# Performance work log

Hardware: AMD Instinct MI355X
Metric: run time of the kernel (lower is better)

## Reference

```python
import jax, jax.numpy as jnp
import numpy as np

THR1 = 0.8     # lif1 threshold
THR2 = 1.0     # lif2 (Synaptic) default threshold
ALPHA2 = 0.9   # Synaptic alpha (not learnable, use_stdp=False)
BETA2 = 0.8    # Synaptic beta
SLOPE = 25.0   # snntorch fast_sigmoid default slope

@jax.custom_vjp
def fast_sigmoid_spike(x):
    return (x > 0).astype(x.dtype)

def _fs_fwd(x):
    return fast_sigmoid_spike(x), x

def _fs_bwd(x, g):
    return (g / (SLOPE * jnp.abs(x) + 1.0) ** 2,)

fast_sigmoid_spike.defvjp(_fs_fwd, _fs_bwd)

@jax.custom_vjp
def atan_spike(x):  # snntorch default ATan surrogate, alpha=2.0
    return (x > 0).astype(x.dtype)

def _at_fwd(x):
    return atan_spike(x), x

def _at_bwd(x, g):
    return (g / (1.0 + (jnp.pi * x) ** 2),)

atan_spike.defvjp(_at_fwd, _at_bwd)

def setup_inputs() -> dict:
    key = jax.random.key(0)
    k = jax.random.split(key, 6)
    B, S, V, H, E, T = 16, 16, 16000, 512, 256, 20
    x = jax.random.randint(k[0], (B, S), 0, V)
    embed_w = jax.random.normal(k[1], (V, E), dtype=jnp.float32)  # torch Embedding ~ N(0,1)
    fc1_w = jax.random.normal(k[2], (H, E), dtype=jnp.float32) / np.sqrt(E)
    fc1_b = jax.random.normal(k[3], (H,), dtype=jnp.float32) / np.sqrt(E)
    fc2_w = jax.random.normal(k[4], (V, H), dtype=jnp.float32) / np.sqrt(H)
    fc2_b = jax.random.normal(k[5], (V,), dtype=jnp.float32) / np.sqrt(H)
    beta1 = jnp.float32(0.85)  # learnable Leaky beta
    return {"x": x, "embed_w": embed_w, "fc1_w": fc1_w, "fc1_b": fc1_b,
            "fc2_w": fc2_w, "fc2_b": fc2_b, "beta1": beta1, "time_steps": T}

def reference(x, embed_w, fc1_w, fc1_b, fc2_w, fc2_b, beta1, time_steps):
    B, S = x.shape
    H = fc1_w.shape[0]
    V = fc2_w.shape[0]
    emb = embed_w[x]                       # [B, S, 256]
    b1 = jnp.clip(beta1, 0.0, 1.0)
    mem1 = jnp.zeros((B, H), emb.dtype)
    syn2 = jnp.zeros((B, V), emb.dtype)
    mem2 = jnp.zeros((B, V), emb.dtype)

    def token_step(carry, emb_t):          # emb_t: [B, 256]
        mem1, syn2, mem2 = carry
        cur1 = emb_t @ fc1_w.T + fc1_b     # identical every inner step (hoisted)

        def inner(c, _):
            m1, s2, m2, _ = c
            reset = fast_sigmoid_spike(m1 - THR1)          # reset from previous mem
            m1 = b1 * m1 + cur1 - reset * THR1             # Leaky, subtract reset
            spk1 = fast_sigmoid_spike(m1 - THR1)
            cur2 = spk1 @ fc2_w.T + fc2_b                  # [B, V]
            s2 = ALPHA2 * s2 + cur2                        # Synaptic, reset='none'
            m2 = BETA2 * m2 + s2
            spk2 = atan_spike(m2 - THR2)
            return (m1, s2, m2, spk2), None

        (mem1, syn2, mem2, spk2), _ = jax.lax.scan(
            inner, (mem1, syn2, mem2, jnp.zeros_like(mem2)), None, length=time_steps)
        return (mem1, syn2, mem2), spk2    # keep last spk2 of inner loop

    (mem1, syn2, mem2), outs = jax.lax.scan(
        token_step, (mem1, syn2, mem2), jnp.swapaxes(emb, 0, 1))  # scan over seq
    out = jnp.transpose(outs, (1, 0, 2))   # [B, S, V]
    return out, mem1, syn2, mem2
```

## Files before the change

kernel.cpp:

```cpp
#include <hip/hip_runtime.h>

#define Bdim 16
#define Sdim 16
#define Edim 256
#define Hdim 512
#define Vdim 16000
#define THR1f 0.8f
#define THR2f 1.0f

typedef unsigned int   u32;
typedef unsigned short u16;
typedef __attribute__((ext_vector_type(8))) short bf16x8;
typedef __attribute__((ext_vector_type(4))) float f32x4;

__device__ __forceinline__ u16 f2bf(float f) {
  u32 u = __float_as_uint(f);
  return (u16)((u + 0x7FFFu + ((u >> 16) & 1u)) >> 16);
}
__device__ __forceinline__ u32 pack2(float a, float b) {
  return (u32)f2bf(a) | ((u32)f2bf(b) << 16);
}
__device__ __forceinline__ void gload16(const void* g, const void* lds) {
  __builtin_amdgcn_global_load_lds(
      (const __attribute__((address_space(1))) u32*)g,
      (__attribute__((address_space(3))) u32*)lds, 16, 0, 0);
}

__global__ __launch_bounds__(256) void snn_cur1(
    const int* __restrict__ x, const float* __restrict__ embed_w,
    const float* __restrict__ fc1_w, const float* __restrict__ fc1_b,
    float* __restrict__ cur1)
{
  __shared__ __align__(16) float As[64][68];
  __shared__ __align__(16) float Ws[64][68];
  __shared__ int sidx[64];
  const int tid = threadIdx.x;
  const int n0 = blockIdx.x * 64, r0 = blockIdx.y * 64;
  const int tx = tid & 15, ty = tid >> 4;

  if (tid < 64) {
    const int r1 = r0 + tid;
    sidx[tid] = x[(r1 & 15) * Sdim + (r1 >> 4)];
  }

  float acc[4][4] = {{0.f}};
  for (int k0 = 0; k0 < Edim; k0 += 64) {
    __syncthreads();
#pragma unroll
    for (int i = 0; i < 16; ++i) {
      const int k = tid + i * 256;
      const int rr = k >> 6, j = k & 63;
      As[j][rr] = embed_w[(size_t)sidx[rr] * Edim + k0 + j];
      Ws[j][rr] = fc1_w[(size_t)(n0 + rr) * Edim + k0 + j];
    }
    __syncthreads();
#pragma unroll
    for (int j = 0; j < 64; ++j) {
      const float4 av = *(const float4*)&As[j][ty * 4];
      const float4 wv = *(const float4*)&Ws[j][tx * 4];
      const float a[4] = {av.x, av.y, av.z, av.w};
      const float w[4] = {wv.x, wv.y, wv.z, wv.w};
#pragma unroll
      for (int i = 0; i < 4; ++i)
#pragma unroll
        for (int jj = 0; jj < 4; ++jj)
          acc[i][jj] = fmaf(a[i], w[jj], acc[i][jj]);
    }
  }
#pragma unroll
  for (int i = 0; i < 4; ++i) {
    float4 o;
    o.x = acc[i][0] + fc1_b[n0 + tx * 4 + 0];
    o.y = acc[i][1] + fc1_b[n0 + tx * 4 + 1];
    o.z = acc[i][2] + fc1_b[n0 + tx * 4 + 2];
    o.w = acc[i][3] + fc1_b[n0 + tx * 4 + 3];
    *(float4*)&cur1[(size_t)(r0 + ty * 4 + i) * Hdim + n0 + tx * 4] = o;
  }
}

__global__ __launch_bounds__(256) void snn_rec(
    const float* __restrict__ cur1, const float* __restrict__ beta1p,
    const int* __restrict__ tsp, u16* __restrict__ Ab,
    float* __restrict__ mem1)
{
  const int id = blockIdx.x * 256 + threadIdx.x;
  const int b = id >> 9, h = id & 511;
  const float b1 = fminf(fmaxf(beta1p[0], 0.f), 1.f);
  const int T = tsp[0];

  double w9T = 1.0, w8T = 1.0;
  for (int i = 0; i < T; ++i) { w9T *= 0.9; w8T *= 0.8; }

  float m1 = 0.f;
  for (int t = 0; t < Sdim; ++t) {
    const float cur = cur1[(size_t)(t * Bdim + b) * Hdim + h];
    double p9 = w9T, p8 = w8T;
    float cs = 0.f, cm = 0.f;
    for (int u = 0; u < T; ++u) {
      const float reset = (m1 > THR1f) ? THR1f : 0.f;
      m1 = b1 * m1 + cur - reset;
      if (m1 > THR1f) {
        cs += (float)(p9 * (10.0 / 9.0));
        cm += (float)(10.0 * (p9 - p8));
      }
      p9 *= (10.0 / 9.0);
      p8 *= 1.25;
    }
    const size_t r = (size_t)(t * Bdim + b) * 2;
    Ab[r * Hdim + h]       = f2bf(cs);
    Ab[(r + 1) * Hdim + h] = f2bf(cm);
  }
  mem1[b * Hdim + h] = m1;
}

__global__ __launch_bounds__(256) void snn_fused(
    const u16* __restrict__ Ab, const float* __restrict__ W,
    const float* __restrict__ fc2_b, const int* __restrict__ tsp,
    float* __restrict__ out, float* __restrict__ syn2, float* __restrict__ mem2)
{
  __shared__ __align__(16) u16 As[512 * 64];
  __shared__ __align__(16) u16 Bs[64 * 64];
  const int tid  = threadIdx.x;
  const int lane = tid & 63;
  const int wid  = tid >> 6;
  const int v0   = blockIdx.x * 64;

  f32x4 acc[32];
#pragma unroll
  for (int i = 0; i < 32; ++i)
#pragma unroll
    for (int e = 0; e < 4; ++e) acc[i][e] = 0.f;

  char* AsB = (char*)As;
  char* BsB = (char*)Bs;

  const int brow = tid >> 2;
  const int bkc  = (tid & 3) * 16;
  const int bswz = (brow & 7) << 4;

  for (int k0 = 0; k0 < Hdim; k0 += 64) {
#pragma unroll
    for (int rnd = 0; rnd < 16; ++rnd) {
      const int base = rnd * 4096 + wid * 1024;
      const int flat = base + lane * 16;
      const int row  = flat >> 7;
      const int cl   = (flat & 127) ^ ((row & 7) << 4);
      gload16(Ab + ((size_t)row << 9) + k0 + (cl >> 1), AsB + base);
    }
    {
      const float4* wp =
          (const float4*)&W[(size_t)(v0 + brow) * Hdim + k0 + bkc];
      const float4 w0 = wp[0], w1 = wp[1], w2 = wp[2], w3 = wp[3];
      uint4 o0, o1;
      o0.x = pack2(w0.x, w0.y); o0.y = pack2(w0.z, w0.w);
      o0.z = pack2(w1.x, w1.y); o0.w = pack2(w1.z, w1.w);
      o1.x = pack2(w2.x, w2.y); o1.y = pack2(w2.z, w2.w);
      o1.z = pack2(w3.x, w3.y); o1.w = pack2(w3.z, w3.w);
      const int cb = bkc * 2;
      *(uint4*)(BsB + brow * 128 + (cb ^ bswz)) = o0;
      *(uint4*)(BsB + brow * 128 + ((cb + 16) ^ bswz)) = o1;
    }
    __syncthreads();
#pragma unroll
    for (int kk = 0; kk < 2; ++kk) {
      const int cbase = kk * 64 + ((lane >> 4) << 4);
      const int br = wid * 16 + (lane & 15);
      const bf16x8 bfr =
          *(const bf16x8*)(BsB + br * 128 + (cbase ^ ((br & 7) << 4)));
#pragma unroll
      for (int mi = 0; mi < 32; ++mi) {
        const int ar = mi * 16 + (lane & 15);
        const bf16x8 af =
            *(const bf16x8*)(AsB + ar * 128 + (cbase ^ ((ar & 7) << 4)));
        acc[mi] = __builtin_amdgcn_mfma_f32_16x16x32_bf16(af, bfr, acc[mi],
                                                          0, 0, 0);
      }
    }
    __syncthreads();
  }

  const int T = tsp[0];
  double p9 = 1.0, p8 = 1.0;
  for (int i = 0; i < T; ++i) { p9 *= 0.9; p8 *= 0.8; }
  const float Ps  = (float)p9;
  const float Pm  = (float)p8;
  const float Pms = (float)(0.9 * 10.0 * (p9 - p8));
  const float Sws = (float)(10.0 * (1.0 - p9));
  const float Swm = (float)(10.0 * (9.0 * (1.0 - p9) - 4.0 * (1.0 - p8)));

  const int g = lane >> 4;
  const int v = v0 + wid * 16 + (lane & 15);
  const float bb  = fc2_b[v];
  const float bbs = bb * Sws;
  const float bbm = bb * Swm;

#pragma unroll
  for (int hi = 0; hi < 2; ++hi) {
#pragma unroll
    for (int j = 0; j < 2; ++j) {
      const int b = hi * 8 + 2 * g + j;
      float s2 = 0.f, m2 = 0.f;
#pragma unroll
      for (int t = 0; t < Sdim; ++t) {
        const float gs = acc[2 * t + hi][2 * j];
        const float gm = acc[2 * t + hi][2 * j + 1];
        const float m2n = Pm * m2 + Pms * s2 + gm + bbm;
        s2 = Ps * s2 + gs + bbs;
        m2 = m2n;
        out[((size_t)b * Sdim + t) * Vdim + v] = (m2 > THR2f) ? 1.f : 0.f;
      }
      syn2[(size_t)b * Vdim + v] = s2;
      mem2[(size_t)b * Vdim + v] = m2;
    }
  }
}

extern "C" void kernel_launch(void* const* d_in, const int* in_sizes, int n_in,
                              void* d_out, int out_size, void* d_ws, size_t ws_size,
                              hipStream_t stream) {
  const int*   x       = (const int*)d_in[0];
  const float* embed_w = (const float*)d_in[1];
  const float* fc1_w   = (const float*)d_in[2];
  const float* fc1_b   = (const float*)d_in[3];
  const float* fc2_w   = (const float*)d_in[4];
  const float* fc2_b   = (const float*)d_in[5];
  const float* beta1   = (const float*)d_in[6];
  const int*   tsteps  = (const int*)d_in[7];

  float* out  = (float*)d_out;
  float* mem1 = out + (size_t)Bdim * Sdim * Vdim;
  float* syn2 = mem1 + (size_t)Bdim * Hdim;
  float* mem2 = syn2 + (size_t)Bdim * Vdim;

  float* cur1 = (float*)d_ws;
  u16*   Ab   = (u16*)((char*)d_ws + 524288);

  snn_cur1<<<dim3(Hdim / 64, (Sdim * Bdim) / 64), 256, 0, stream>>>(
      x, embed_w, fc1_w, fc1_b, cur1);
  snn_rec<<<(Bdim * Hdim) / 256, 256, 0, stream>>>(cur1, beta1, tsteps, Ab, mem1);
  snn_fused<<<Vdim / 64, 256, 0, stream>>>(Ab, fc2_w, fc2_b, tsteps,
                                           out, syn2, mem2);
}
```

Before: 156.3 us.

## Double-buffer fused GEMM, use 32x32 MFMA with 8 waves splitting M

Rewrites the fused fc2 GEMM kernel to use 512 threads (8 waves), each computing a 64x64 M-slice with 32x32x16 bf16 MFMAs. A and B tiles are double-buffered in LDS so the next k-chunk's global loads overlap the current MFMAs, and the per-iteration barrier count drops to one. Because time steps are now split across waves, the synaptic recurrence epilogue is serialized through LDS state handoff across 8 barrier stages. The aim is to cut register pressure from the 32 accumulators and hide load latency, but LDS use roughly doubles and the epilogue becomes sequential across waves.

Result: no change. 157.7 us (+0.9%).

```diff
diff --git a/kernel.cpp b/kernel.cpp
--- a/kernel.cpp
+++ b/kernel.cpp
@@ -10,8 +10,8 @@
 
 typedef unsigned int   u32;
 typedef unsigned short u16;
-typedef __attribute__((ext_vector_type(8))) short bf16x8;
-typedef __attribute__((ext_vector_type(4))) float f32x4;
+typedef __attribute__((ext_vector_type(8)))  short bf16x8;
+typedef __attribute__((ext_vector_type(16))) float f32x16;
 
 __device__ __forceinline__ u16 f2bf(float f) {
   u32 u = __float_as_uint(f);
@@ -113,70 +113,97 @@
   mem1[b * Hdim + h] = m1;
 }
 
-__global__ __launch_bounds__(256) void snn_fused(
+__global__ __launch_bounds__(512, 2) void snn_fused(
     const u16* __restrict__ Ab, const float* __restrict__ W,
     const float* __restrict__ fc2_b, const int* __restrict__ tsp,
     float* __restrict__ out, float* __restrict__ syn2, float* __restrict__ mem2)
 {
-  __shared__ __align__(16) u16 As[512 * 64];
-  __shared__ __align__(16) u16 Bs[64 * 64];
+  __shared__ __align__(16) u16 AsBuf[2][512 * 64];
+  __shared__ __align__(16) u16 BsBuf[2][64 * 64];
+  __shared__ float2 stbuf[16 * 64];
   const int tid  = threadIdx.x;
   const int lane = tid & 63;
-  const int wid  = tid >> 6;
+  const int wm   = tid >> 6;
   const int v0   = blockIdx.x * 64;
 
-  f32x4 acc[32];
-#pragma unroll
-  for (int i = 0; i < 32; ++i)
-#pragma unroll
-    for (int e = 0; e < 4; ++e) acc[i][e] = 0.f;
-
-  char* AsB = (char*)As;
-  char* BsB = (char*)Bs;
-
-  const int brow = tid >> 2;
-  const int bkc  = (tid & 3) * 16;
-  const int bswz = (brow & 7) << 4;
-
+  f32x16 acc[2][2];
+#pragma unroll
+  for (int mi = 0; mi < 2; ++mi)
+#pragma unroll
+    for (int nj = 0; nj < 2; ++nj)
+#pragma unroll
+      for (int e = 0; e < 16; ++e) acc[mi][nj][e] = 0.f;
+
+  const int brow = tid >> 3;
+  const int bk8  = (tid & 7) * 8;
+  const int bdst = brow * 128 + (((tid & 7) * 16) ^ ((brow & 7) << 4));
+
+#define STAGE_A(buf, k0s)                                                    \
+  {                                                                          \
+    _Pragma("unroll")                                                        \
+    for (int rnd = 0; rnd < 8; ++rnd) {                                      \
+      const int base = rnd * 8192 + (wm << 10);            \
+      const int flat = base + lane * 16;                                     \
+      const int row  = flat >> 7;                                            \
+      const int cl   = (flat & 127) ^ ((row & 7) << 4);                      \
+      gload16(Ab + ((size_t)row << 9) + (k0s) + (cl >> 1),                   \
+              (char*)AsBuf[buf] + base);                                     \
+    }                                                                        \
+  }
+
+  STAGE_A(0, 0);
+  {
+    const float4* wp = (const float4*)&W[(size_t)(v0 + brow) * Hdim + bk8];
+    const float4 wa = wp[0], wb = wp[1];
+    uint4 o;
+    o.x = pack2(wa.x, wa.y); o.y = pack2(wa.z, wa.w);
+    o.z = pack2(wb.x, wb.y); o.w = pack2(wb.z, wb.w);
+    *(uint4*)((char*)BsBuf[0] + bdst) = o;
+  }
+  __syncthreads();
+
+  int c = 0;
   for (int k0 = 0; k0 < Hdim; k0 += 64) {
-#pragma unroll
-    for (int rnd = 0; rnd < 16; ++rnd) {
-      const int base = rnd * 4096 + wid * 1024;
-      const int flat = base + lane * 16;
-      const int row  = flat >> 7;
-      const int cl   = (flat & 127) ^ ((row & 7) << 4);
-      gload16(Ab + ((size_t)row << 9) + k0 + (cl >> 1), AsB + base);
-    }
-    {
+    float4 wa, wb;
+    const bool pf = (k0 + 64 < Hdim);
+    if (pf) {
+      STAGE_A(c ^ 1, k0 + 64);
       const float4* wp =
-          (const float4*)&W[(size_t)(v0 + brow) * Hdim + k0 + bkc];
-      const float4 w0 = wp[0], w1 = wp[1], w2 = wp[2], w3 = wp[3];
-      uint4 o0, o1;
-      o0.x = pack2(w0.x, w0.y); o0.y = pack2(w0.z, w0.w);
-      o0.z = pack2(w1.x, w1.y); o0.w = pack2(w1.z, w1.w);
-      o1.x = pack2(w2.x, w2.y); o1.y = pack2(w2.z, w2.w);
-      o1.z = pack2(w3.x, w3.y); o1.w = pack2(w3.z, w3.w);
-      const int cb = bkc * 2;
-      *(uint4*)(BsB + brow * 128 + (cb ^ bswz)) = o0;
-      *(uint4*)(BsB + brow * 128 + ((cb + 16) ^ bswz)) = o1;
+          (const float4*)&W[(size_t)(v0 + brow) * Hdim + (k0 + 64) + bk8];
+      wa = wp[0]; wb = wp[1];
+    }
+    const int h16 = (lane >> 5) * 16;
+#pragma unroll
+    for (int kk = 0; kk < 4; ++kk) {
+      const int cb = kk * 32 + h16;
+      bf16x8 bfr[2], afr[2];
+#pragma unroll
+      for (int nj = 0; nj < 2; ++nj) {
+        const int br = nj * 32 + (lane & 31);
+        bfr[nj] = *(const bf16x8*)((char*)BsBuf[c] + br * 128 +
+                                   (cb ^ ((br & 7) << 4)));
+      }
+#pragma unroll
+      for (int mi = 0; mi < 2; ++mi) {
+        const int ar = wm * 64 + mi * 32 + (lane & 31);
+        afr[mi] = *(const bf16x8*)((char*)AsBuf[c] + ar * 128 +
+                                   (cb ^ ((ar & 7) << 4)));
+      }
+#pragma unroll
+      for (int mi = 0; mi < 2; ++mi)
+#pragma unroll
+        for (int nj = 0; nj < 2; ++nj)
+          acc[mi][nj] = __builtin_amdgcn_mfma_f32_32x32x16_bf16(
+              afr[mi], bfr[nj], acc[mi][nj], 0, 0, 0);
+    }
+    if (pf) {
+      uint4 o;
+      o.x = pack2(wa.x, wa.y); o.y = pack2(wa.z, wa.w);
+      o.z = pack2(wb.x, wb.y); o.w = pack2(wb.z, wb.w);
+      *(uint4*)((char*)BsBuf[c ^ 1] + bdst) = o;
     }
     __syncthreads();
-#pragma unroll
-    for (int kk = 0; kk < 2; ++kk) {
-      const int cbase = kk * 64 + ((lane >> 4) << 4);
-      const int br = wid * 16 + (lane & 15);
-      const bf16x8 bfr =
-          *(const bf16x8*)(BsB + br * 128 + (cbase ^ ((br & 7) << 4)));
-#pragma unroll
-      for (int mi = 0; mi < 32; ++mi) {
-        const int ar = mi * 16 + (lane & 15);
-        const bf16x8 af =
-            *(const bf16x8*)(AsB + ar * 128 + (cbase ^ ((ar & 7) << 4)));
-        acc[mi] = __builtin_amdgcn_mfma_f32_16x16x32_bf16(af, bfr, acc[mi],
-                                                          0, 0, 0);
-      }
-    }
-    __syncthreads();
+    c ^= 1;
   }
 
   const int T = tsp[0];
@@ -188,30 +215,72 @@
   const float Sws = (float)(10.0 * (1.0 - p9));
   const float Swm = (float)(10.0 * (9.0 * (1.0 - p9) - 4.0 * (1.0 - p8)));
 
-  const int g = lane >> 4;
-  const int v = v0 + wid * 16 + (lane & 15);
-  const float bb  = fc2_b[v];
-  const float bbs = bb * Sws;
-  const float bbm = bb * Swm;
-
-#pragma unroll
-  for (int hi = 0; hi < 2; ++hi) {
-#pragma unroll
-    for (int j = 0; j < 2; ++j) {
-      const int b = hi * 8 + 2 * g + j;
-      float s2 = 0.f, m2 = 0.f;
-#pragma unroll
-      for (int t = 0; t < Sdim; ++t) {
-        const float gs = acc[2 * t + hi][2 * j];
-        const float gm = acc[2 * t + hi][2 * j + 1];
-        const float m2n = Pm * m2 + Pms * s2 + gm + bbm;
-        s2 = Ps * s2 + gs + bbs;
-        m2 = m2n;
-        out[((size_t)b * Sdim + t) * Vdim + v] = (m2 > THR2f) ? 1.f : 0.f;
+  const int h  = lane >> 5;
+  const int vl = lane & 31;
+  float bbs[2], bbm[2];
+#pragma unroll
+  for (int nj = 0; nj < 2; ++nj) {
+    const float bb = fc2_b[v0 + nj * 32 + vl];
+    bbs[nj] = bb * Sws;
+    bbm[nj] = bb * Swm;
+  }
+
+  float s2[2][8], m2[2][8];
+  for (int s = 0; s < 8; ++s) {
+    if (wm == s) {
+#pragma unroll
+      for (int nj = 0; nj < 2; ++nj)
+#pragma unroll
+        for (int rq = 0; rq < 4; ++rq)
+#pragma unroll
+          for (int j = 0; j < 2; ++j) {
+            const int b = j + 4 * rq + 2 * h;
+            if (s > 0) {
+              const float2 st = stbuf[b * 64 + nj * 32 + vl];
+              s2[nj][rq * 2 + j] = st.x; m2[nj][rq * 2 + j] = st.y;
+            } else {
+              s2[nj][rq * 2 + j] = 0.f; m2[nj][rq * 2 + j] = 0.f;
+            }
+          }
+#pragma unroll
+      for (int mi = 0; mi < 2; ++mi) {
+        const int t = 2 * s + mi;
+#pragma unroll
+        for (int nj = 0; nj < 2; ++nj)
+#pragma unroll
+          for (int rq = 0; rq < 4; ++rq)
+#pragma unroll
+            for (int j = 0; j < 2; ++j) {
+              const int b  = j + 4 * rq + 2 * h;
+              const int si = rq * 2 + j;
+              const float gs = acc[mi][nj][4 * rq + 2 * j];
+              const float gm = acc[mi][nj][4 * rq + 2 * j + 1];
+              const float m2n =
+                  Pm * m2[nj][si] + Pms * s2[nj][si] + gm + bbm[nj];
+              s2[nj][si] = Ps * s2[nj][si] + gs + bbs[nj];
+              m2[nj][si] = m2n;
+              out[((size_t)b * Sdim + t) * Vdim + v0 + nj * 32 + vl] =
+                  (m2n > THR2f) ? 1.f : 0.f;
+            }
       }
-      syn2[(size_t)b * Vdim + v] = s2;
-      mem2[(size_t)b * Vdim + v] = m2;
-    }
+#pragma unroll
+      for (int nj = 0; nj < 2; ++nj)
+#pragma unroll
+        for (int rq = 0; rq < 4; ++rq)
+#pragma unroll
+          for (int j = 0; j < 2; ++j) {
+            const int b  = j + 4 * rq + 2 * h;
+            const int si = rq * 2 + j;
+            if (s < 7) {
+              stbuf[b * 64 + nj * 32 + vl] =
+                  make_float2(s2[nj][si], m2[nj][si]);
+            } else {
+              syn2[(size_t)b * Vdim + v0 + nj * 32 + vl] = s2[nj][si];
+              mem2[(size_t)b * Vdim + v0 + nj * 32 + vl] = m2[nj][si];
+            }
+          }
+    }
+    __syncthreads();
   }
 }
 
@@ -238,6 +307,6 @@
   snn_cur1<<<dim3(Hdim / 64, (Sdim * Bdim) / 64), 256, 0, stream>>>(
       x, embed_w, fc1_w, fc1_b, cur1);
   snn_rec<<<(Bdim * Hdim) / 256, 256, 0, stream>>>(cur1, beta1, tsteps, Ab, mem1);
-  snn_fused<<<Vdim / 64, 256, 0, stream>>>(Ab, fc2_w, fc2_b, tsteps,
+  snn_fused<<<Vdim / 64, 512, 0, stream>>>(Ab, fc2_w, fc2_b, tsteps,
                                            out, syn2, mem2);
 }
```

## Fuse cur1 GEMM with LIF recurrence and pre-swizzle A into MFMA fragment layout

Applied to the files above, without the earlier changes.

Merges the cur1 GEMM and the layer-1 recurrence into a single prep kernel that keeps cur1 in LDS, so the workspace round trip and one launch go away. The prep kernel writes the spike-weighted A operand straight into MFMA fragment order, which lets the main kernel read A fragments directly from global/L2 and drop the LDS staging and barriers. Each lane loads its own fc2 weights into registers with a one-step prefetch and converts them to bf16 there. The price is that prep now runs only 32 blocks, and every V-block rereads the full A from L2.

Result: slower. 174.9 us (+11.9%).

```diff
diff --git a/kernel.cpp b/kernel.cpp
--- a/kernel.cpp
+++ b/kernel.cpp
@@ -12,6 +12,7 @@
 typedef unsigned short u16;
 typedef __attribute__((ext_vector_type(8))) short bf16x8;
 typedef __attribute__((ext_vector_type(4))) float f32x4;
+typedef __attribute__((ext_vector_type(4))) u32   u32x4;
 
 __device__ __forceinline__ u16 f2bf(float f) {
   u32 u = __float_as_uint(f);
@@ -20,28 +21,23 @@
 __device__ __forceinline__ u32 pack2(float a, float b) {
   return (u32)f2bf(a) | ((u32)f2bf(b) << 16);
 }
-__device__ __forceinline__ void gload16(const void* g, const void* lds) {
-  __builtin_amdgcn_global_load_lds(
-      (const __attribute__((address_space(1))) u32*)g,
-      (__attribute__((address_space(3))) u32*)lds, 16, 0, 0);
-}
-
-__global__ __launch_bounds__(256) void snn_cur1(
+
+__global__ __launch_bounds__(256) void snn_prep(
     const int* __restrict__ x, const float* __restrict__ embed_w,
     const float* __restrict__ fc1_w, const float* __restrict__ fc1_b,
-    float* __restrict__ cur1)
+    const float* __restrict__ beta1p, const int* __restrict__ tsp,
+    u16* __restrict__ Ab3, float* __restrict__ mem1)
 {
   __shared__ __align__(16) float As[64][68];
   __shared__ __align__(16) float Ws[64][68];
+  __shared__ float cbuf[64][68];
   __shared__ int sidx[64];
   const int tid = threadIdx.x;
-  const int n0 = blockIdx.x * 64, r0 = blockIdx.y * 64;
+  const int n0  = blockIdx.x * 64;
+  const int bi0 = blockIdx.y * 4;
   const int tx = tid & 15, ty = tid >> 4;
 
-  if (tid < 64) {
-    const int r1 = r0 + tid;
-    sidx[tid] = x[(r1 & 15) * Sdim + (r1 >> 4)];
-  }
+  if (tid < 64) sidx[tid] = x[(bi0 + (tid & 3)) * Sdim + (tid >> 2)];
 
   float acc[4][4] = {{0.f}};
   for (int k0 = 0; k0 < Edim; k0 += 64) {
@@ -68,32 +64,26 @@
     }
   }
 #pragma unroll
-  for (int i = 0; i < 4; ++i) {
-    float4 o;
-    o.x = acc[i][0] + fc1_b[n0 + tx * 4 + 0];
-    o.y = acc[i][1] + fc1_b[n0 + tx * 4 + 1];
-    o.z = acc[i][2] + fc1_b[n0 + tx * 4 + 2];
-    o.w = acc[i][3] + fc1_b[n0 + tx * 4 + 3];
-    *(float4*)&cur1[(size_t)(r0 + ty * 4 + i) * Hdim + n0 + tx * 4] = o;
-  }
-}
-
-__global__ __launch_bounds__(256) void snn_rec(
-    const float* __restrict__ cur1, const float* __restrict__ beta1p,
-    const int* __restrict__ tsp, u16* __restrict__ Ab,
-    float* __restrict__ mem1)
-{
-  const int id = blockIdx.x * 256 + threadIdx.x;
-  const int b = id >> 9, h = id & 511;
+  for (int i = 0; i < 4; ++i)
+#pragma unroll
+    for (int jj = 0; jj < 4; ++jj)
+      cbuf[ty * 4 + i][tx * 4 + jj] = acc[i][jj] + fc1_b[n0 + tx * 4 + jj];
+  __syncthreads();
+
+  const int bb = tid >> 6, hl = tid & 63;
+  const int b  = bi0 + bb;
+  const int hg = n0 + hl;
   const float b1 = fminf(fmaxf(beta1p[0], 0.f), 1.f);
   const int T = tsp[0];
 
   double w9T = 1.0, w8T = 1.0;
   for (int i = 0; i < T; ++i) { w9T *= 0.9; w8T *= 0.8; }
 
+  const int S = hg >> 5, q = (hg >> 3) & 3, jc = hg & 7;
+
   float m1 = 0.f;
   for (int t = 0; t < Sdim; ++t) {
-    const float cur = cur1[(size_t)(t * Bdim + b) * Hdim + h];
+    const float cur = cbuf[t * 4 + bb][hl];
     double p9 = w9T, p8 = w8T;
     float cs = 0.f, cm = 0.f;
     for (int u = 0; u < T; ++u) {
@@ -106,77 +96,55 @@
       p9 *= (10.0 / 9.0);
       p8 *= 1.25;
     }
-    const size_t r = (size_t)(t * Bdim + b) * 2;
-    Ab[r * Hdim + h]       = f2bf(cs);
-    Ab[(r + 1) * Hdim + h] = f2bf(cm);
-  }
-  mem1[b * Hdim + h] = m1;
-}
-
-__global__ __launch_bounds__(256) void snn_fused(
-    const u16* __restrict__ Ab, const float* __restrict__ W,
+    int rb = 2 * b;
+    int R  = 2 * t + (rb >> 4);
+    int l  = q * 16 + (rb & 15);
+    Ab3[((size_t)(S * 32 + R) * 64 + l) * 8 + jc] = f2bf(cs);
+    rb = 2 * b + 1;
+    R  = 2 * t + (rb >> 4);
+    l  = q * 16 + (rb & 15);
+    Ab3[((size_t)(S * 32 + R) * 64 + l) * 8 + jc] = f2bf(cm);
+  }
+  mem1[b * Hdim + hg] = m1;
+}
+
+__global__ __launch_bounds__(256, 1) void snn_fused(
+    const u16* __restrict__ Ab3, const float* __restrict__ W,
     const float* __restrict__ fc2_b, const int* __restrict__ tsp,
     float* __restrict__ out, float* __restrict__ syn2, float* __restrict__ mem2)
 {
-  __shared__ __align__(16) u16 As[512 * 64];
-  __shared__ __align__(16) u16 Bs[64 * 64];
   const int tid  = threadIdx.x;
   const int lane = tid & 63;
-  const int wid  = tid >> 6;
+  const int wn   = tid >> 6;
   const int v0   = blockIdx.x * 64;
+  const int v    = v0 + wn * 16 + (lane & 15);
 
   f32x4 acc[32];
 #pragma unroll
-  for (int i = 0; i < 32; ++i)
-#pragma unroll
-    for (int e = 0; e < 4; ++e) acc[i][e] = 0.f;
-
-  char* AsB = (char*)As;
-  char* BsB = (char*)Bs;
-
-  const int brow = tid >> 2;
-  const int bkc  = (tid & 3) * 16;
-  const int bswz = (brow & 7) << 4;
-
-  for (int k0 = 0; k0 < Hdim; k0 += 64) {
-#pragma unroll
-    for (int rnd = 0; rnd < 16; ++rnd) {
-      const int base = rnd * 4096 + wid * 1024;
-      const int flat = base + lane * 16;
-      const int row  = flat >> 7;
-      const int cl   = (flat & 127) ^ ((row & 7) << 4);
-      gload16(Ab + ((size_t)row << 9) + k0 + (cl >> 1), AsB + base);
-    }
-    {
-      const float4* wp =
-          (const float4*)&W[(size_t)(v0 + brow) * Hdim + k0 + bkc];
-      const float4 w0 = wp[0], w1 = wp[1], w2 = wp[2], w3 = wp[3];
-      uint4 o0, o1;
-      o0.x = pack2(w0.x, w0.y); o0.y = pack2(w0.z, w0.w);
-      o0.z = pack2(w1.x, w1.y); o0.w = pack2(w1.z, w1.w);
-      o1.x = pack2(w2.x, w2.y); o1.y = pack2(w2.z, w2.w);
-      o1.z = pack2(w3.x, w3.y); o1.w = pack2(w3.z, w3.w);
-      const int cb = bkc * 2;
-      *(uint4*)(BsB + brow * 128 + (cb ^ bswz)) = o0;
-      *(uint4*)(BsB + brow * 128 + ((cb + 16) ^ bswz)) = o1;
-    }
-    __syncthreads();
-#pragma unroll
-    for (int kk = 0; kk < 2; ++kk) {
-      const int cbase = kk * 64 + ((lane >> 4) << 4);
-      const int br = wid * 16 + (lane & 15);
-      const bf16x8 bfr =
-          *(const bf16x8*)(BsB + br * 128 + (cbase ^ ((br & 7) << 4)));
-#pragma unroll
-      for (int mi = 0; mi < 32; ++mi) {
-        const int ar = mi * 16 + (lane & 15);
-        const bf16x8 af =
-            *(const bf16x8*)(AsB + ar * 128 + (cbase ^ ((ar & 7) << 4)));
-        acc[mi] = __builtin_amdgcn_mfma_f32_16x16x32_bf16(af, bfr, acc[mi],
-                                                          0, 0, 0);
-      }
-    }
-    __syncthreads();
+  for (int R = 0; R < 32; ++R)
+#pragma unroll
+    for (int e = 0; e < 4; ++e) acc[R][e] = 0.f;
+
+  const float* wrow = W + (size_t)v * Hdim + ((lane >> 4) * 8);
+  float4 wa = *(const float4*)(wrow);
+  float4 wb = *(const float4*)(wrow + 4);
+
+  for (int S = 0; S < 16; ++S) {
+    const int Sn = (S + 1) & 15;
+    const float4 na = *(const float4*)(wrow + Sn * 32);
+    const float4 nb = *(const float4*)(wrow + Sn * 32 + 4);
+    u32x4 bw;
+    bw.x = pack2(wa.x, wa.y); bw.y = pack2(wa.z, wa.w);
+    bw.z = pack2(wb.x, wb.y); bw.w = pack2(wb.z, wb.w);
+    const bf16x8 bfr = __builtin_bit_cast(bf16x8, bw);
+    const char* abase = (const char*)Ab3 + (size_t)S * 32768 + lane * 16;
+#pragma unroll
+    for (int R = 0; R < 32; ++R) {
+      const bf16x8 af = *(const bf16x8*)(abase + R * 1024);
+      acc[R] = __builtin_amdgcn_mfma_f32_16x16x32_bf16(af, bfr, acc[R],
+                                                       0, 0, 0);
+    }
+    wa = na; wb = nb;
   }
 
   const int T = tsp[0];
@@ -189,10 +157,9 @@
   const float Swm = (float)(10.0 * (9.0 * (1.0 - p9) - 4.0 * (1.0 - p8)));
 
   const int g = lane >> 4;
-  const int v = v0 + wid * 16 + (lane & 15);
-  const float bb  = fc2_b[v];
-  const float bbs = bb * Sws;
-  const float bbm = bb * Swm;
+  const float bbv = fc2_b[v];
+  const float bbs = bbv * Sws;
+  const float bbm = bbv * Swm;
 
 #pragma unroll
   for (int hi = 0; hi < 2; ++hi) {
@@ -207,7 +174,7 @@
         const float m2n = Pm * m2 + Pms * s2 + gm + bbm;
         s2 = Ps * s2 + gs + bbs;
         m2 = m2n;
-        out[((size_t)b * Sdim + t) * Vdim + v] = (m2 > THR2f) ? 1.f : 0.f;
+        out[((size_t)b * Sdim + t) * Vdim + v] = (m2n > THR2f) ? 1.f : 0.f;
       }
       syn2[(size_t)b * Vdim + v] = s2;
       mem2[(size_t)b * Vdim + v] = m2;
@@ -232,12 +199,10 @@
   float* syn2 = mem1 + (size_t)Bdim * Hdim;
   float* mem2 = syn2 + (size_t)Bdim * Vdim;
 
-  float* cur1 = (float*)d_ws;
-  u16*   Ab   = (u16*)((char*)d_ws + 524288);
-
-  snn_cur1<<<dim3(Hdim / 64, (Sdim * Bdim) / 64), 256, 0, stream>>>(
-      x, embed_w, fc1_w, fc1_b, cur1);
-  snn_rec<<<(Bdim * Hdim) / 256, 256, 0, stream>>>(cur1, beta1, tsteps, Ab, mem1);
-  snn_fused<<<Vdim / 64, 256, 0, stream>>>(Ab, fc2_w, fc2_b, tsteps,
+  u16* Ab3 = (u16*)d_ws;
+
+  snn_prep<<<dim3(8, 4), 256, 0, stream>>>(x, embed_w, fc1_w, fc1_b,
+                                           beta1, tsteps, Ab3, mem1);
+  snn_fused<<<Vdim / 64, 256, 0, stream>>>(Ab3, fc2_w, fc2_b, tsteps,
                                            out, syn2, mem2);
 }
```
